# Optimization experiments

Measured on AMD Instinct MI355X. Metric: run time of the kernel, lower is better.

## Reference

```python
import jax, jax.numpy as jnp
import numpy as np

N = 50000
DEG = 16
E = N * DEG
IN_F, HID, OUT_F = 512, 128, 64
SLOPE = 0.2


def setup_inputs() -> dict:
    key = jax.random.key(0)
    ks = jax.random.split(key, 10)
    row_ptr = jnp.arange(N + 1, dtype=jnp.int64) * DEG          # uniform-degree CSR
    col_idx = jax.random.randint(ks[0], (E,), 0, N, dtype=jnp.int64)
    x = jax.random.normal(ks[1], (N, IN_F), dtype=jnp.float32)
    s1 = 1.0 / np.sqrt(IN_F)
    s2 = 1.0 / np.sqrt(HID)
    return {
        "row_ptr": row_ptr,
        "col_idx": col_idx,
        "input_feature": x,
        "W1": jax.random.normal(ks[2], (IN_F, HID), dtype=jnp.float32) * s1,
        "attn_l1": jax.random.normal(ks[3], (HID,), dtype=jnp.float32) * s2,
        "attn_r1": jax.random.normal(ks[4], (HID,), dtype=jnp.float32) * s2,
        "bias1": jnp.zeros((HID,), dtype=jnp.float32),
        "W2": jax.random.normal(ks[5], (HID, OUT_F), dtype=jnp.float32) * s2,
        "attn_l2": jax.random.normal(ks[6], (OUT_F,), dtype=jnp.float32) * 0.125,
        "attn_r2": jax.random.normal(ks[7], (OUT_F,), dtype=jnp.float32) * 0.125,
        "bias2": jnp.zeros((OUT_F,), dtype=jnp.float32),
    }


def gat_layer(row_ptr, col_idx, x, W, attn_l, attn_r, bias):
    n = row_ptr.shape[0] - 1
    e = col_idx.shape[0]
    h = x @ W                                   # [N, F] dense GEMM
    el = h @ attn_l                             # [N] dst attention term
    er = h @ attn_r                             # [N] src attention term
    # edge -> destination row via CSR row_ptr
    dst = jnp.searchsorted(row_ptr, jnp.arange(e, dtype=row_ptr.dtype), side="right") - 1
    src = col_idx
    score = jax.nn.leaky_relu(el[dst] + er[src], negative_slope=SLOPE)  # [E]
    # neighborhood softmax over edges sharing a destination
    smax = jax.ops.segment_max(score, dst, num_segments=n)
    ex = jnp.exp(score - smax[dst])
    ssum = jax.ops.segment_sum(ex, dst, num_segments=n)
    alpha = ex / ssum[dst]                      # [E]
    # weighted gather-scatter aggregation
    out = jax.ops.segment_sum(alpha[:, None] * h[src], dst, num_segments=n)
    return out + bias


def reference(row_ptr, col_idx, input_feature, W1, attn_l1, attn_r1, bias1,
              W2, attn_l2, attn_r2, bias2):
    x = gat_layer(row_ptr, col_idx, input_feature, W1, attn_l1, attn_r1, bias1)
    x = gat_layer(row_ptr, col_idx, x, W2, attn_l2, attn_r2, bias2)
    return x
```

## Files before the change

### kernel.cpp

```cpp
#include <hip/hip_runtime.h>
#include <hip/hip_bf16.h>

#define Nn 50000
#define DEG 16
#define IN_F 512
#define HID 128
#define OUT_F 64
#define SLOPE 0.2f

typedef __attribute__((ext_vector_type(8))) short bf16x8;
typedef __attribute__((ext_vector_type(4))) float f32x4;
typedef __attribute__((ext_vector_type(4))) unsigned int u32x4;

__device__ __forceinline__ unsigned short f2bf(float f) {
    return __builtin_bit_cast(unsigned short, __float2bfloat16(f));
}
__device__ __forceinline__ float bf2f(unsigned short u) {
    return __bfloat162float(__builtin_bit_cast(__hip_bfloat16, u));
}
__device__ __forceinline__ void async_copy16(const void* g, void* l) {
    __builtin_amdgcn_global_load_lds(
        (const __attribute__((address_space(1))) unsigned int*)g,
        (__attribute__((address_space(3))) unsigned int*)l, 16, 0, 0);
}

__global__ void __launch_bounds__(256) prep_kernel(
        const float* __restrict__ W1, const float* __restrict__ W2,
        const float* __restrict__ al1, const float* __restrict__ ar1,
        const float* __restrict__ b1, const int* __restrict__ row_ptr,
        unsigned short* __restrict__ w12c, float* __restrict__ uv,
        float* __restrict__ c2v, int* __restrict__ flag64) {
    const int tid = threadIdx.x;
    const int lane = tid & 63;
    const int w = tid >> 6;
    const int k = blockIdx.x * 4 + w;
    if (blockIdx.x == 0 && tid == 0) {
        *flag64 = (row_ptr[1] == DEG) ? 0 : 1;
    }
    const float* w1row = W1 + (size_t)k * HID;

    float acc = 0.f;
    #pragma unroll 8
    for (int j = 0; j < HID; ++j)
        acc += w1row[j] * W2[j * OUT_F + lane];
    {
        int ch = k >> 7, kin = k & 127;
        int bsrc = kin >> 3, j = kin & 7;
        int bdst = bsrc ^ (lane & 7);
        w12c[ch * 8192 + lane * 128 + bdst * 8 + j] = f2bf(acc);
    }

    float pu = w1row[lane] * al1[lane] + w1row[lane + 64] * al1[lane + 64];
    float pv = w1row[lane] * ar1[lane] + w1row[lane + 64] * ar1[lane + 64];
    #pragma unroll
    for (int m = 1; m < 64; m <<= 1) {
        pu += __shfl_xor(pu, m);
        pv += __shfl_xor(pv, m);
    }
    if (lane == 0) { uv[k] = pu; uv[IN_F + k] = pv; }

    if (blockIdx.x == 0 && w == 0) {
        float cacc = 0.f;
        #pragma unroll 8
        for (int j = 0; j < HID; ++j) cacc += b1[j] * W2[j * OUT_F + lane];
        c2v[lane] = cacc;
    }
}

template<int K>
__global__ void __launch_bounds__(256) gemm1_tiled(
        const float* __restrict__ Af, const unsigned short* __restrict__ w12c,
        const float* __restrict__ uv,
        unsigned short* __restrict__ G, float* __restrict__ el,
        float* __restrict__ er, int M) {
    constexpr int NCH = K / 128;
    __shared__ float As[64 * 128];
    __shared__ unsigned short Bs[64 * 128];

    const int tid  = threadIdx.x;
    const int lane = tid & 63;
    const int w    = tid >> 6;
    const int ln   = lane & 15, q = lane >> 4;
    const int r2   = lane >> 5, b = lane & 31;
    const int mb   = blockIdx.x * 64;

    f32x4 acc[4] = {};
    float sl = 0.f, sr = 0.f;

    for (int ch = 0; ch < NCH; ++ch) {
        const char* gb = (const char*)w12c + ch * 16384;
        #pragma unroll
        for (int i = 0; i < 4; ++i) {
            int slot = w * 4 + i;
            async_copy16(gb + slot * 1024 + lane * 16, (char*)Bs + slot * 1024);
        }
        #pragma unroll
        for (int i = 0; i < 8; ++i) {
            int rl = w * 16 + i * 2 + r2;
            int rg = mb + rl; if (rg > M - 1) rg = M - 1;
            int c  = rl & 7;
            const float* src = Af + (size_t)rg * K + ch * 128 + ((b ^ c) << 2);
            async_copy16(src, (char*)As + (size_t)(w * 16 + i * 2) * 512);
        }
        __syncthreads();

        const float* up = uv + ch * 128;
        const float* vp = uv + K + ch * 128;
        const int c = ln & 7;
        #pragma unroll
        for (int ks = 0; ks < 4; ++ks) {
            const int b0 = ks * 8 + q * 2;
            f32x4 a0 = *(const f32x4*)&As[(w * 16 + ln) * 128 + ((b0 ^ c) << 2)];
            f32x4 a1 = *(const f32x4*)&As[(w * 16 + ln) * 128 + (((b0 + 1) ^ c) << 2)];
            f32x4 u0 = *(const f32x4*)(up + ks * 32 + q * 8);
            f32x4 u1 = *(const f32x4*)(up + ks * 32 + q * 8 + 4);
            f32x4 v0 = *(const f32x4*)(vp + ks * 32 + q * 8);
            f32x4 v1 = *(const f32x4*)(vp + ks * 32 + q * 8 + 4);
            bf16x8 af;
            #pragma unroll
            for (int jj = 0; jj < 4; ++jj) {
                af[jj]     = (short)f2bf(a0[jj]);
                af[jj + 4] = (short)f2bf(a1[jj]);
                sl += a0[jj] * u0[jj] + a1[jj] * u1[jj];
                sr += a0[jj] * v0[jj] + a1[jj] * v1[jj];
            }
            #pragma unroll
            for (int nt = 0; nt < 4; ++nt) {
                const int bb = ks * 4 + q;
                bf16x8 bfr = *(const bf16x8*)&Bs[(nt * 16 + ln) * 128 + ((bb ^ c) << 3)];
                acc[nt] = __builtin_amdgcn_mfma_f32_16x16x32_bf16(af, bfr, acc[nt], 0, 0, 0);
            }
        }
        __syncthreads();
    }

    sl += __shfl_xor(sl, 16); sl += __shfl_xor(sl, 32);
    sr += __shfl_xor(sr, 16); sr += __shfl_xor(sr, 32);
    const int rowe = mb + w * 16 + ln;
    if (q == 0 && rowe < M) { el[rowe] = sl; er[rowe] = sr; }

    #pragma unroll
    for (int r = 0; r < 4; ++r) {
        int grow = mb + w * 16 + q * 4 + r;
        if (grow < M) {
            #pragma unroll
            for (int nt = 0; nt < 4; ++nt)
                G[(size_t)grow * OUT_F + nt * 16 + ln] = f2bf(acc[nt][r]);
        }
    }
}

template<int MODE>
__global__ void __launch_bounds__(256) agg_k(
        const int* __restrict__ col, const int* __restrict__ flag64,
        const float* __restrict__ el, const float* __restrict__ er,
        const unsigned short* __restrict__ Hs, const float* __restrict__ addv,
        const float* __restrict__ alv, const float* __restrict__ arv,
        unsigned short* __restrict__ Ho, float* __restrict__ elo,
        float* __restrict__ ero, float* __restrict__ Fo) {
    const int tid  = threadIdx.x;
    const int lane = tid & 63;
    const int w    = tid >> 6;
    const int ln   = lane & 15, q = lane >> 4;
    const int g16  = w * 4 + q;
    const int nA   = blockIdx.x * 32 + g16 * 2;
    const int nB   = nA + 1;
    const int nAc  = nA < Nn ? nA : Nn - 1;
    const int nBc  = nB < Nn ? nB : Nn - 1;
    const int use64 = *flag64;

    int eA = nAc * DEG + ln, eB = nBc * DEG + ln;
    int srcA = use64 ? (int)((const long long*)col)[eA] : col[eA];
    int srcB = use64 ? (int)((const long long*)col)[eB] : col[eB];
    float scA = el[nAc] + er[srcA];
    float scB = el[nBc] + er[srcB];
    scA = scA >= 0.f ? scA : SLOPE * scA;
    scB = scB >= 0.f ? scB : SLOPE * scB;
    float mxA = scA, mxB = scB;
    #pragma unroll
    for (int m = 1; m < 16; m <<= 1) {
        mxA = fmaxf(mxA, __shfl_xor(mxA, m, 16));
        mxB = fmaxf(mxB, __shfl_xor(mxB, m, 16));
    }
    float exA = __expf(scA - mxA), exB = __expf(scB - mxB);
    float smA = exA, smB = exB;
    #pragma unroll
    for (int m = 1; m < 16; m <<= 1) {
        smA += __shfl_xor(smA, m, 16);
        smB += __shfl_xor(smB, m, 16);
    }
    float alA = exA / smA, alB = exB / smB;

    const int half = ln >> 3, cc = ln & 7;
    float aA[8] = {}, aB[8] = {};
    #pragma unroll
    for (int jj = 0; jj < DEG; jj += 2) {
        int   sjA = __shfl(srcA, jj + half, 16);
        float ajA = __shfl(alA,  jj + half, 16);
        int   sjB = __shfl(srcB, jj + half, 16);
        float ajB = __shfl(alB,  jj + half, 16);
        bf16x8 hA = *(const bf16x8*)&Hs[(size_t)sjA * OUT_F + cc * 8];
        bf16x8 hB = *(const bf16x8*)&Hs[(size_t)sjB * OUT_F + cc * 8];
        #pragma unroll
        for (int c = 0; c < 8; ++c) {
            aA[c] += ajA * bf2f((unsigned short)hA[c]);
            aB[c] += ajB * bf2f((unsigned short)hB[c]);
        }
    }
    #pragma unroll
    for (int c = 0; c < 8; ++c) {
        aA[c] += __shfl_xor(aA[c], 8, 16);
        aB[c] += __shfl_xor(aB[c], 8, 16);
        float ad = addv[cc * 8 + c];
        aA[c] += ad;
        aB[c] += ad;
    }

    if (MODE == 0) {
        float plA = 0.f, prA = 0.f, plB = 0.f, prB = 0.f;
        #pragma unroll
        for (int c = 0; c < 8; ++c) {
            float av = alv[cc * 8 + c], bv = arv[cc * 8 + c];
            plA += aA[c] * av;  prA += aA[c] * bv;
            plB += aB[c] * av;  prB += aB[c] * bv;
        }
        #pragma unroll
        for (int m = 1; m < 8; m <<= 1) {
            plA += __shfl_xor(plA, m, 16);  prA += __shfl_xor(prA, m, 16);
            plB += __shfl_xor(plB, m, 16);  prB += __shfl_xor(prB, m, 16);
        }
        if (ln == 0) {
            if (nA < Nn) { elo[nA] = plA; ero[nA] = prA; }
            if (nB < Nn) { elo[nB] = plB; ero[nB] = prB; }
        }
        if (half == 0) {
            unsigned int pkA[4], pkB[4];
            #pragma unroll
            for (int c = 0; c < 4; ++c) {
                pkA[c] = (unsigned int)f2bf(aA[2 * c]) |
                         ((unsigned int)f2bf(aA[2 * c + 1]) << 16);
                pkB[c] = (unsigned int)f2bf(aB[2 * c]) |
                         ((unsigned int)f2bf(aB[2 * c + 1]) << 16);
            }
            if (nA < Nn) *(u32x4*)&Ho[(size_t)nA * OUT_F + cc * 8] = *(u32x4*)pkA;
            if (nB < Nn) *(u32x4*)&Ho[(size_t)nB * OUT_F + cc * 8] = *(u32x4*)pkB;
        }
    } else {
        if (half == 0) {
            f32x4 oA0, oA1, oB0, oB1;
            #pragma unroll
            for (int c = 0; c < 4; ++c) {
                oA0[c] = aA[c]; oA1[c] = aA[c + 4];
                oB0[c] = aB[c]; oB1[c] = aB[c + 4];
            }
            if (nA < Nn) {
                *(f32x4*)&Fo[(size_t)nA * OUT_F + cc * 8]     = oA0;
                *(f32x4*)&Fo[(size_t)nA * OUT_F + cc * 8 + 4] = oA1;
            }
            if (nB < Nn) {
                *(f32x4*)&Fo[(size_t)nB * OUT_F + cc * 8]     = oB0;
                *(f32x4*)&Fo[(size_t)nB * OUT_F + cc * 8 + 4] = oB1;
            }
        }
    }
}

extern "C" void kernel_launch(void* const* d_in, const int* in_sizes, int n_in,
                              void* d_out, int out_size, void* d_ws, size_t ws_size,
                              hipStream_t stream) {
    const int*   row_ptr = (const int*)d_in[0];
    const int*   col_idx = (const int*)d_in[1];
    const float* x   = (const float*)d_in[2];
    const float* W1  = (const float*)d_in[3];
    const float* al1 = (const float*)d_in[4];
    const float* ar1 = (const float*)d_in[5];
    const float* b1  = (const float*)d_in[6];
    const float* W2  = (const float*)d_in[7];
    const float* al2 = (const float*)d_in[8];
    const float* ar2 = (const float*)d_in[9];
    const float* b2  = (const float*)d_in[10];
    float* out = (float*)d_out;

    float* ws = (float*)d_ws;
    unsigned short* g   = (unsigned short*)ws;
    unsigned short* h2b = (unsigned short*)(ws + 1600000);
    float* el1 = ws + 3200000;
    float* er1 = ws + 3250000;
    float* el2 = ws + 3300000;
    float* er2 = ws + 3350000;
    unsigned short* w12c = (unsigned short*)(ws + 3400000);
    float* uv  = ws + 3420000;
    float* c2v = ws + 3421024;
    int* flag64 = (int*)(ws + 3421100);

    prep_kernel<<<128, 256, 0, stream>>>(
        W1, W2, al1, ar1, b1, row_ptr, w12c, uv, c2v, flag64);

    gemm1_tiled<IN_F><<<(Nn + 63) / 64, 256, 0, stream>>>(
        x, w12c, uv, g, el1, er1, Nn);

    agg_k<0><<<(Nn + 31) / 32, 256, 0, stream>>>(
        col_idx, flag64, el1, er1, g, c2v, al2, ar2, h2b, el2, er2, nullptr);

    agg_k<1><<<(Nn + 31) / 32, 256, 0, stream>>>(
        col_idx, flag64, el2, er2, h2b, b2, nullptr, nullptr,
        nullptr, nullptr, nullptr, out);
}
```

Before: 223.3 us.

## Double-buffer GEMM1 K-chunks and batch neighbor gathers in aggregation

GEMM1 now uses 64-wide K chunks with two LDS buffers, so the async copy of the next chunk is issued before the MFMAs on the current one, and it caches the uv attention vectors in shared memory. The prep kernel's swizzled W12 layout is changed to match the 64-wide chunks. The aggregation kernel issues all eight neighbor row gathers up front before accumulating, to expose more memory-level parallelism. The costs are more register pressure in the aggregation and a barrier that still sits on every chunk, and the whole thing is bound by the x read from HBM.

```diff
diff --git a/kernel.cpp b/kernel.cpp
--- a/kernel.cpp
+++ b/kernel.cpp
@@ -44,10 +44,10 @@
     for (int j = 0; j < HID; ++j)
         acc += w1row[j] * W2[j * OUT_F + lane];
     {
-        int ch = k >> 7, kin = k & 127;
+        int ch = k >> 6, kin = k & 63;
         int bsrc = kin >> 3, j = kin & 7;
         int bdst = bsrc ^ (lane & 7);
-        w12c[ch * 8192 + lane * 128 + bdst * 8 + j] = f2bf(acc);
+        w12c[ch * 4096 + lane * 64 + bdst * 8 + j] = f2bf(acc);
     }
 
     float pu = w1row[lane] * al1[lane] + w1row[lane + 64] * al1[lane + 64];
@@ -68,54 +68,63 @@
 }
 
 template<int K>
-__global__ void __launch_bounds__(256) gemm1_tiled(
+__global__ void __launch_bounds__(256) gemm1_pipe(
         const float* __restrict__ Af, const unsigned short* __restrict__ w12c,
         const float* __restrict__ uv,
         unsigned short* __restrict__ G, float* __restrict__ el,
         float* __restrict__ er, int M) {
-    constexpr int NCH = K / 128;
-    __shared__ float As[64 * 128];
-    __shared__ unsigned short Bs[64 * 128];
+    constexpr int NCH = K / 64;
+    __shared__ float As[2][64 * 64];
+    __shared__ unsigned short Bs[2][64 * 64];
+    __shared__ float uvs[2 * K];
 
     const int tid  = threadIdx.x;
     const int lane = tid & 63;
     const int w    = tid >> 6;
     const int ln   = lane & 15, q = lane >> 4;
-    const int r2   = lane >> 5, b = lane & 31;
     const int mb   = blockIdx.x * 64;
+
+    *(f32x4*)&uvs[tid * 4] = *(const f32x4*)&uv[tid * 4];
+
+    auto stage = [&](int buf, int ch) {
+        const char* gb = (const char*)w12c + ch * 8192;
+        #pragma unroll
+        for (int i = 0; i < 2; ++i) {
+            int slot = w * 2 + i;
+            async_copy16(gb + slot * 1024 + lane * 16,
+                         (char*)&Bs[buf][0] + slot * 1024);
+        }
+        #pragma unroll
+        for (int i = 0; i < 4; ++i) {
+            int slot = w * 4 + i;
+            int rl = slot * 4 + (lane >> 4);
+            int rg = mb + rl; if (rg > M - 1) rg = M - 1;
+            int b  = lane & 15;
+            const float* src = Af + (size_t)rg * K + ch * 64 + ((b ^ (rl & 7)) << 2);
+            async_copy16(src, (char*)&As[buf][0] + slot * 1024);
+        }
+    };
 
     f32x4 acc[4] = {};
     float sl = 0.f, sr = 0.f;
 
+    stage(0, 0);
+    __syncthreads();
+
+    int buf = 0;
     for (int ch = 0; ch < NCH; ++ch) {
-        const char* gb = (const char*)w12c + ch * 16384;
-        #pragma unroll
-        for (int i = 0; i < 4; ++i) {
-            int slot = w * 4 + i;
-            async_copy16(gb + slot * 1024 + lane * 16, (char*)Bs + slot * 1024);
-        }
-        #pragma unroll
-        for (int i = 0; i < 8; ++i) {
-            int rl = w * 16 + i * 2 + r2;
-            int rg = mb + rl; if (rg > M - 1) rg = M - 1;
-            int c  = rl & 7;
-            const float* src = Af + (size_t)rg * K + ch * 128 + ((b ^ c) << 2);
-            async_copy16(src, (char*)As + (size_t)(w * 16 + i * 2) * 512);
-        }
-        __syncthreads();
-
-        const float* up = uv + ch * 128;
-        const float* vp = uv + K + ch * 128;
-        const int c = ln & 7;
-        #pragma unroll
-        for (int ks = 0; ks < 4; ++ks) {
+        if (ch + 1 < NCH) stage(buf ^ 1, ch + 1);
+
+        const int c7 = ln & 7;
+        #pragma unroll
+        for (int ks = 0; ks < 2; ++ks) {
             const int b0 = ks * 8 + q * 2;
-            f32x4 a0 = *(const f32x4*)&As[(w * 16 + ln) * 128 + ((b0 ^ c) << 2)];
-            f32x4 a1 = *(const f32x4*)&As[(w * 16 + ln) * 128 + (((b0 + 1) ^ c) << 2)];
-            f32x4 u0 = *(const f32x4*)(up + ks * 32 + q * 8);
-            f32x4 u1 = *(const f32x4*)(up + ks * 32 + q * 8 + 4);
-            f32x4 v0 = *(const f32x4*)(vp + ks * 32 + q * 8);
-            f32x4 v1 = *(const f32x4*)(vp + ks * 32 + q * 8 + 4);
+            f32x4 a0 = *(const f32x4*)&As[buf][(w * 16 + ln) * 64 + ((b0 ^ c7) << 2)];
+            f32x4 a1 = *(const f32x4*)&As[buf][(w * 16 + ln) * 64 + (((b0 + 1) ^ c7) << 2)];
+            f32x4 u0 = *(const f32x4*)&uvs[ch * 64 + ks * 32 + q * 8];
+            f32x4 u1 = *(const f32x4*)&uvs[ch * 64 + ks * 32 + q * 8 + 4];
+            f32x4 v0 = *(const f32x4*)&uvs[K + ch * 64 + ks * 32 + q * 8];
+            f32x4 v1 = *(const f32x4*)&uvs[K + ch * 64 + ks * 32 + q * 8 + 4];
             bf16x8 af;
             #pragma unroll
             for (int jj = 0; jj < 4; ++jj) {
@@ -127,11 +136,12 @@
             #pragma unroll
             for (int nt = 0; nt < 4; ++nt) {
                 const int bb = ks * 4 + q;
-                bf16x8 bfr = *(const bf16x8*)&Bs[(nt * 16 + ln) * 128 + ((bb ^ c) << 3)];
+                bf16x8 bfr = *(const bf16x8*)&Bs[buf][(nt * 16 + ln) * 64 + ((bb ^ c7) << 3)];
                 acc[nt] = __builtin_amdgcn_mfma_f32_16x16x32_bf16(af, bfr, acc[nt], 0, 0, 0);
             }
         }
         __syncthreads();
+        buf ^= 1;
     }
 
     sl += __shfl_xor(sl, 16); sl += __shfl_xor(sl, 32);
@@ -192,19 +202,23 @@
     float alA = exA / smA, alB = exB / smB;
 
     const int half = ln >> 3, cc = ln & 7;
+    bf16x8 hA[8], hB[8];
+    #pragma unroll
+    for (int p = 0; p < 8; ++p) {
+        int sjA = __shfl(srcA, p * 2 + half, 16);
+        int sjB = __shfl(srcB, p * 2 + half, 16);
+        hA[p] = *(const bf16x8*)&Hs[(size_t)sjA * OUT_F + cc * 8];
+        hB[p] = *(const bf16x8*)&Hs[(size_t)sjB * OUT_F + cc * 8];
+    }
     float aA[8] = {}, aB[8] = {};
     #pragma unroll
-    for (int jj = 0; jj < DEG; jj += 2) {
-        int   sjA = __shfl(srcA, jj + half, 16);
-        float ajA = __shfl(alA,  jj + half, 16);
-        int   sjB = __shfl(srcB, jj + half, 16);
-        float ajB = __shfl(alB,  jj + half, 16);
-        bf16x8 hA = *(const bf16x8*)&Hs[(size_t)sjA * OUT_F + cc * 8];
-        bf16x8 hB = *(const bf16x8*)&Hs[(size_t)sjB * OUT_F + cc * 8];
+    for (int p = 0; p < 8; ++p) {
+        float wA = __shfl(alA, p * 2 + half, 16);
+        float wB = __shfl(alB, p * 2 + half, 16);
         #pragma unroll
         for (int c = 0; c < 8; ++c) {
-            aA[c] += ajA * bf2f((unsigned short)hA[c]);
-            aB[c] += ajB * bf2f((unsigned short)hB[c]);
+            aA[c] += wA * bf2f((unsigned short)hA[p][c]);
+            aB[c] += wB * bf2f((unsigned short)hB[p][c]);
         }
     }
     #pragma unroll
@@ -296,7 +310,7 @@
     prep_kernel<<<128, 256, 0, stream>>>(
         W1, W2, al1, ar1, b1, row_ptr, w12c, uv, c2v, flag64);
 
-    gemm1_tiled<IN_F><<<(Nn + 63) / 64, 256, 0, stream>>>(
+    gemm1_pipe<IN_F><<<(Nn + 63) / 64, 256, 0, stream>>>(
         x, w12c, uv, g, el1, er1, Nn);
 
     agg_k<0><<<(Nn + 31) / 32, 256, 0, stream>>>(
```

New measurement: 224.9 us. Within noise of the previous version (+0.7%).
